# Kernel optimization log

Hardware: AMD Instinct MI355X
Metric: run time of the kernel (lower is better)

The kernel has to match this reference:

```python
import jax, jax.numpy as jnp
import numpy as np

B, N, H, OUT, T = 8192, 82, 10, 5, 3  # batch, n_nodes, hidden, output_channel, time_step


def setup_inputs() -> dict:
    key = jax.random.key(0)
    ks = jax.random.split(key, 20)

    def lin(kw, kb, fin, fout):
        w = jax.random.normal(kw, (fout, fin), jnp.float32) * (1.0 / np.sqrt(fin))
        b = jax.random.normal(kb, (fout,), jnp.float32) * 0.01
        return w, b

    w3w, b3w = lin(ks[0], ks[1], 2 * H, H)
    w3u, b3u = lin(ks[2], ks[3], H, H)
    w4w, b4w = lin(ks[4], ks[5], 2 * H, H)
    w5w, b5w = lin(ks[6], ks[7], 2 * H, H)
    w5u, b5u = lin(ks[8], ks[9], H, H)
    wout, bout = lin(ks[10], ks[11], 2 * H, OUT)
    return {
        'x': jax.random.normal(ks[12], (B, N, H), jnp.float32),
        'in_adj': jax.random.uniform(ks[13], (N, N), jnp.float32),
        'out_adj': jax.random.uniform(ks[14], (N, N), jnp.float32),
        'w3w': w3w, 'b3w': b3w, 'w3u': w3u, 'b3u': b3u,
        'w4w': w4w, 'b4w': b4w, 'w5w': w5w, 'b5w': b5w,
        'w5u': w5u, 'b5u': b5u, 'wout': wout, 'bout': bout,
    }


def _dense(v, w, b):
    return v @ w.T + b


def reference(x, in_adj, out_adj, w3w, b3w, w3u, b3u, w4w, b4w,
              w5w, b5w, w5u, b5u, wout, bout):
    b, n, h = x.shape
    nodes = x  # [B, N, H]
    fn = nodes.reshape(b * n, h)
    for _ in range(T):
        # neighbor aggregation; adjacency shared across batch (torch tiles it with repeat)
        a_in = jnp.einsum('ij,bjh->bih', in_adj, nodes)
        a_out = jnp.einsum('ij,bjh->bih', out_adj, nodes)
        av = jnp.concatenate([a_in, a_out], axis=-1).reshape(b * n, 2 * h)
        fn = nodes.reshape(b * n, h)
        zv = jax.nn.sigmoid(_dense(av, w3w, b3w) + _dense(fn, w3u, b3u))
        # NOTE: original torch code (bug) reuses fc_eq3_u here instead of fc_eq4_u
        rv = jax.nn.sigmoid(_dense(av, w4w, b4w) + _dense(fn, w3u, b3u))
        hv = jnp.tanh(_dense(av, w5w, b5w) + _dense(rv * fn, w5u, b5u))
        fn = (1.0 - zv) * fn + zv * hv
        nodes = fn.reshape(b, n, h)
    out_in = jnp.concatenate([fn, x.reshape(b * n, h)], axis=1)
    output = jnp.tanh(_dense(out_in, wout, bout))
    return output, fn
```

## Files before the change

kernel.cpp:

```cpp
#include <hip/hip_runtime.h>
#include <hip/hip_bf16.h>
#include <math.h>

#define B_TOTAL 8192
#define NN      82
#define HH      10
#define OUTC    5
#define TSTEP   3
#define NB      3
#define THREADS 256
#define KP      96
#define MP      16
#define XS      104
#define UTS     248

#define W3W 0
#define W4W 200
#define W5W 400
#define W3U 600
#define W5U 700
#define WOUT 800
#define B3W 900
#define B4W 910
#define B5W 920
#define B3U 930
#define B5U 940
#define BOUT 950
#define WTOT 960

typedef __bf16 bf16x8 __attribute__((ext_vector_type(8)));
typedef float  f32x4  __attribute__((ext_vector_type(4)));
typedef float  f32x2  __attribute__((ext_vector_type(2)));

__device__ __forceinline__ float sigmoid_(float x) {
    return 1.0f / (1.0f + __expf(-x));
}
__device__ __forceinline__ float tanh_(float x) {
    float e = __expf(2.0f * x);
    return 1.0f - 2.0f / (e + 1.0f);
}
__device__ __forceinline__ f32x2 ld2(const float* p) {
    return *reinterpret_cast<const f32x2*>(p);
}
__device__ __forceinline__ f32x2 fma2(f32x2 a, f32x2 b, f32x2 c) {
    return __builtin_elementwise_fma(a, b, c);
}

__global__ void prep_adj_kernel(const float* __restrict__ in_adj,
                                const float* __restrict__ out_adj,
                                __hip_bfloat16* __restrict__ adjP) {
    int idx = blockIdx.x * blockDim.x + threadIdx.x;
    if (idx < 2 * KP * KP) {
        int a   = idx / (KP * KP);
        int rem = idx - a * (KP * KP);
        int i = rem / KP;
        int j = rem - i * KP;
        float v = 0.0f;
        if (i < NN && j < NN) v = (a == 0) ? in_adj[i * NN + j] : out_adj[i * NN + j];
        __hip_bfloat16 hi = __float2bfloat16(v);
        __hip_bfloat16 lo = __float2bfloat16(v - __bfloat162float(hi));
        adjP[idx]               = hi;
        adjP[2 * KP * KP + idx] = lo;
    }
}

extern "C" __global__ __launch_bounds__(THREADS, 3)
void ggnn_kernel(const float* __restrict__ x,
                 const __hip_bfloat16* __restrict__ adjP,
                 const float* __restrict__ w3w, const float* __restrict__ b3w,
                 const float* __restrict__ w3u, const float* __restrict__ b3u,
                 const float* __restrict__ w4w, const float* __restrict__ b4w,
                 const float* __restrict__ w5w, const float* __restrict__ b5w,
                 const float* __restrict__ w5u, const float* __restrict__ b5u,
                 const float* __restrict__ wout, const float* __restrict__ bout,
                 float* __restrict__ out0, float* __restrict__ out_fn)
{
    __shared__ __align__(16) __hip_bfloat16 XtH[NB * MP][XS];
    __shared__ __align__(16) __hip_bfloat16 XtL[NB * MP][XS];
    __shared__ float uinT [HH][UTS];
    __shared__ float uoutT[HH][UTS];
    __shared__ __align__(16) float wS[WTOT];

    const int t     = threadIdx.x;
    const int bbase = blockIdx.x * NB;
    const int bl    = t / NN;
    const int node  = t - bl * NN;
    const bool act  = (bl < NB) && (bbase + bl < B_TOTAL);
    const int b     = bbase + bl;

    const int lane = t & 63;
    const int w    = t >> 6;
    const int lo16 = lane & 15;
    const int quad = lane >> 4;

    for (int i = t; i < 200; i += THREADS) {
        wS[W3W + i] = w3w[i];
        wS[W4W + i] = w4w[i];
        wS[W5W + i] = w5w[i];
    }
    if (t < 100) {
        wS[W3U + t]  = w3u[t];
        wS[W5U + t]  = w5u[t];
        wS[WOUT + t] = wout[t];
    }
    if (t < 10) {
        wS[B3W + t] = b3w[t];
        wS[B4W + t] = b4w[t];
        wS[B5W + t] = b5w[t];
        wS[B3U + t] = b3u[t];
        wS[B5U + t] = b5u[t];
    }
    if (t < OUTC) wS[BOUT + t] = bout[t];

    bf16x8 Bh[3][3], Bl[3][3];
    int ntile_c[3], adj_c[3];
    #pragma unroll
    for (int c = 0; c < 3; ++c) {
        int co = w * 3 + c;
        int nt = co >> 1;
        int ad = co & 1;
        ntile_c[c] = nt;
        adj_c[c]   = ad;
        const __hip_bfloat16* BpH = adjP + ((size_t)ad * KP * KP
                                            + (size_t)(nt * 16 + lo16) * KP
                                            + quad * 8);
        #pragma unroll
        for (int k = 0; k < 3; ++k) {
            Bh[c][k] = *reinterpret_cast<const bf16x8*>(BpH + k * 32);
            Bl[c][k] = *reinterpret_cast<const bf16x8*>(BpH + 2 * KP * KP + k * 32);
        }
    }

    for (int idx = t; idx < NB * NN * HH; idx += THREADS) {
        int b_l = idx / (NN * HH);
        int rem = idx - b_l * (NN * HH);
        int j   = rem / HH;
        int h   = rem - j * HH;
        size_t g = (size_t)bbase * NN * HH + idx;
        float v = (g < (size_t)B_TOTAL * NN * HH) ? x[g] : 0.0f;
        __hip_bfloat16 hi = __float2bfloat16(v);
        __hip_bfloat16 lo = __float2bfloat16(v - __bfloat162float(hi));
        XtH[b_l * MP + h][j] = hi;
        XtL[b_l * MP + h][j] = lo;
    }
    for (int idx = t; idx < NB * MP * (KP - NN); idx += THREADS) {
        int r = idx / (KP - NN);
        int c = idx - r * (KP - NN);
        __hip_bfloat16 z = __float2bfloat16(0.0f);
        XtH[r][NN + c] = z;
        XtL[r][NN + c] = z;
    }

    f32x2 fn2[5];
    if (act) {
        const float* xr = x + ((size_t)b * NN + node) * HH;
        #pragma unroll
        for (int p = 0; p < 5; ++p) {
            float2 v = reinterpret_cast<const float2*>(xr)[p];
            fn2[p].x = v.x; fn2[p].y = v.y;
        }
    }

    #pragma unroll 1
    for (int step = 0; step < TSTEP; ++step) {
        __syncthreads();

        #pragma unroll
        for (int mtile = 0; mtile < NB; ++mtile) {
            f32x4 acc[3] = {{0,0,0,0}, {0,0,0,0}, {0,0,0,0}};
            #pragma unroll
            for (int k = 0; k < 3; ++k) {
                bf16x8 ah = *reinterpret_cast<const bf16x8*>(&XtH[mtile * MP + lo16][quad * 8 + k * 32]);
                bf16x8 al = *reinterpret_cast<const bf16x8*>(&XtL[mtile * MP + lo16][quad * 8 + k * 32]);
                #pragma unroll
                for (int c = 0; c < 3; ++c) {
                    acc[c] = __builtin_amdgcn_mfma_f32_16x16x32_bf16(ah, Bh[c][k], acc[c], 0, 0, 0);
                    acc[c] = __builtin_amdgcn_mfma_f32_16x16x32_bf16(al, Bh[c][k], acc[c], 0, 0, 0);
                    acc[c] = __builtin_amdgcn_mfma_f32_16x16x32_bf16(ah, Bl[c][k], acc[c], 0, 0, 0);
                }
            }
            #pragma unroll
            for (int c = 0; c < 3; ++c) {
                int i = ntile_c[c] * 16 + lo16;
                if (i < NN) {
                    int col = mtile * NN + i;
                    float* plane0 = adj_c[c] ? &uoutT[0][0] : &uinT[0][0];
                    if (quad < 2) {
                        #pragma unroll
                        for (int r = 0; r < 4; ++r)
                            plane0[(quad * 4 + r) * UTS + col] = acc[c][r];
                    } else if (quad == 2) {
                        plane0[8 * UTS + col] = acc[c][0];
                        plane0[9 * UTS + col] = acc[c][1];
                    }
                }
            }
        }

        __syncthreads();

        if (act) {
            f32x2 av2[10];
            #pragma unroll
            for (int p = 0; p < 5; ++p) {
                av2[p].x     = uinT [2 * p][t];
                av2[p].y     = uinT [2 * p + 1][t];
                av2[5 + p].x = uoutT[2 * p][t];
                av2[5 + p].y = uoutT[2 * p + 1][t];
            }

            float u3[HH];
            #pragma unroll
            for (int h = 0; h < HH; ++h) {
                f32x2 s2 = {0.0f, 0.0f};
                #pragma unroll
                for (int p = 0; p < 5; ++p)
                    s2 = fma2(ld2(&wS[W3U + h * HH + 2 * p]), fn2[p], s2);
                u3[h] = wS[B3U + h] + s2.x + s2.y;
            }

            float zv[HH];
            f32x2 rf2[5];
            #pragma unroll
            for (int h = 0; h < HH; ++h) {
                f32x2 z2 = {0.0f, 0.0f}, r2 = {0.0f, 0.0f};
                #pragma unroll
                for (int p = 0; p < 10; ++p) {
                    z2 = fma2(ld2(&wS[W3W + h * 20 + 2 * p]), av2[p], z2);
                    r2 = fma2(ld2(&wS[W4W + h * 20 + 2 * p]), av2[p], r2);
                }
                zv[h] = sigmoid_(wS[B3W + h] + z2.x + z2.y + u3[h]);
                float rv = sigmoid_(wS[B4W + h] + r2.x + r2.y + u3[h]);
                float fnh = (h & 1) ? fn2[h >> 1].y : fn2[h >> 1].x;
                if (h & 1) rf2[h >> 1].y = rv * fnh; else rf2[h >> 1].x = rv * fnh;
            }

            #pragma unroll
            for (int h = 0; h < HH; ++h) {
                f32x2 s2 = {0.0f, 0.0f};
                #pragma unroll
                for (int p = 0; p < 10; ++p)
                    s2 = fma2(ld2(&wS[W5W + h * 20 + 2 * p]), av2[p], s2);
                #pragma unroll
                for (int p = 0; p < 5; ++p)
                    s2 = fma2(ld2(&wS[W5U + h * HH + 2 * p]), rf2[p], s2);
                float hv = tanh_(wS[B5W + h] + wS[B5U + h] + s2.x + s2.y);
                float fnh = (h & 1) ? fn2[h >> 1].y : fn2[h >> 1].x;
                fnh = fnh + zv[h] * (hv - fnh);
                if (h & 1) fn2[h >> 1].y = fnh; else fn2[h >> 1].x = fnh;
            }

            #pragma unroll
            for (int h = 0; h < HH; ++h) {
                float fnh = (h & 1) ? fn2[h >> 1].y : fn2[h >> 1].x;
                __hip_bfloat16 hi = __float2bfloat16(fnh);
                __hip_bfloat16 lo = __float2bfloat16(fnh - __bfloat162float(hi));
                XtH[bl * MP + h][node] = hi;
                XtL[bl * MP + h][node] = lo;
            }
        }
    }

    if (act) {
        size_t row = (size_t)b * NN + node;
        const float* xr = x + row * HH;
        f32x2 xi2[5];
        #pragma unroll
        for (int p = 0; p < 5; ++p) {
            float2 v = reinterpret_cast<const float2*>(xr)[p];
            xi2[p].x = v.x; xi2[p].y = v.y;
        }

        #pragma unroll
        for (int c = 0; c < OUTC; ++c) {
            f32x2 s2 = {0.0f, 0.0f};
            #pragma unroll
            for (int p = 0; p < 5; ++p) {
                s2 = fma2(ld2(&wS[WOUT + c * 20 + 2 * p]),      fn2[p], s2);
                s2 = fma2(ld2(&wS[WOUT + c * 20 + 10 + 2 * p]), xi2[p], s2);
            }
            out0[row * OUTC + c] = tanh_(wS[BOUT + c] + s2.x + s2.y);
        }
        #pragma unroll
        for (int p = 0; p < 5; ++p) {
            reinterpret_cast<float2*>(out_fn + row * HH)[p] =
                make_float2(fn2[p].x, fn2[p].y);
        }
    }
}

extern "C" void kernel_launch(void* const* d_in, const int* in_sizes, int n_in,
                              void* d_out, int out_size, void* d_ws, size_t ws_size,
                              hipStream_t stream) {
    const float* x       = (const float*)d_in[0];
    const float* in_adj  = (const float*)d_in[1];
    const float* out_adj = (const float*)d_in[2];
    const float* w3w = (const float*)d_in[3];
    const float* b3w = (const float*)d_in[4];
    const float* w3u = (const float*)d_in[5];
    const float* b3u = (const float*)d_in[6];
    const float* w4w = (const float*)d_in[7];
    const float* b4w = (const float*)d_in[8];
    const float* w5w = (const float*)d_in[9];
    const float* b5w = (const float*)d_in[10];
    const float* w5u = (const float*)d_in[11];
    const float* b5u = (const float*)d_in[12];
    const float* wout = (const float*)d_in[13];
    const float* bout = (const float*)d_in[14];

    __hip_bfloat16* adjP = (__hip_bfloat16*)d_ws;
    float* out0   = (float*)d_out;
    float* out_fn = out0 + (size_t)B_TOTAL * NN * OUTC;

    prep_adj_kernel<<<(2 * KP * KP + 255) / 256, 256, 0, stream>>>(in_adj, out_adj, adjP);

    int grid = (B_TOTAL + NB - 1) / NB;
    ggnn_kernel<<<grid, THREADS, 0, stream>>>(
        x, adjP, w3w, b3w, w3u, b3u, w4w, b4w, w5w, b5w, w5u, b5u,
        wout, bout, out0, out_fn);
}
```

Measured before the change: 264.6 us.

## Alias shared-memory buffers and pack batch rows to raise occupancy

Puts the bf16 X tiles and the float aggregation planes in one shared byte buffer that they take turns using, and shrinks the per-batch row pitch from 16 to 10. Extra barriers separate the MFMA reads, the aggregate writes and the av loads so the aliased regions do not collide. The accumulators for all m-tiles are now held in registers across the barrier. Launch bounds go from 3 to 6 blocks per CU to use the smaller LDS footprint. The trade-off is more __syncthreads and higher register pressure. The packed rows also make the MFMA A-loads read rows that belong to the neighbouring batch or are uninitialised, and that extra output is simply discarded. The pad-column zeroing has to be redone each step because the float planes overwrite it.

After: 684.0 us. 159% more time.

```diff
diff --git a/kernel.cpp b/kernel.cpp
--- a/kernel.cpp
+++ b/kernel.cpp
@@ -10,9 +10,14 @@
 #define NB      3
 #define THREADS 256
 #define KP      96
-#define MP      16
+#define RS      10
+#define NROWS   36
 #define XS      104
-#define UTS     248
+#define UTSF    246
+
+#define XTL_OFF 7488
+#define WS_OFF  19680
+#define SMEM_BYTES 23520
 
 #define W3W 0
 #define W4W 200
@@ -26,7 +31,6 @@
 #define B3U 930
 #define B5U 940
 #define BOUT 950
-#define WTOT 960
 
 typedef __bf16 bf16x8 __attribute__((ext_vector_type(8)));
 typedef float  f32x4  __attribute__((ext_vector_type(4)));
@@ -64,7 +68,7 @@
     }
 }
 
-extern "C" __global__ __launch_bounds__(THREADS, 3)
+extern "C" __global__ __launch_bounds__(THREADS, 6)
 void ggnn_kernel(const float* __restrict__ x,
                  const __hip_bfloat16* __restrict__ adjP,
                  const float* __restrict__ w3w, const float* __restrict__ b3w,
@@ -75,11 +79,11 @@
                  const float* __restrict__ wout, const float* __restrict__ bout,
                  float* __restrict__ out0, float* __restrict__ out_fn)
 {
-    __shared__ __align__(16) __hip_bfloat16 XtH[NB * MP][XS];
-    __shared__ __align__(16) __hip_bfloat16 XtL[NB * MP][XS];
-    __shared__ float uinT [HH][UTS];
-    __shared__ float uoutT[HH][UTS];
-    __shared__ __align__(16) float wS[WTOT];
+    __shared__ __align__(16) unsigned char smem[SMEM_BYTES];
+    __hip_bfloat16* XtH = reinterpret_cast<__hip_bfloat16*>(smem);
+    __hip_bfloat16* XtL = reinterpret_cast<__hip_bfloat16*>(smem + XTL_OFF);
+    float* uT = reinterpret_cast<float*>(smem);
+    float* wS = reinterpret_cast<float*>(smem + WS_OFF);
 
     const int t     = threadIdx.x;
     const int bbase = blockIdx.x * NB;
@@ -140,15 +144,18 @@
         float v = (g < (size_t)B_TOTAL * NN * HH) ? x[g] : 0.0f;
         __hip_bfloat16 hi = __float2bfloat16(v);
         __hip_bfloat16 lo = __float2bfloat16(v - __bfloat162float(hi));
-        XtH[b_l * MP + h][j] = hi;
-        XtL[b_l * MP + h][j] = lo;
-    }
-    for (int idx = t; idx < NB * MP * (KP - NN); idx += THREADS) {
-        int r = idx / (KP - NN);
-        int c = idx - r * (KP - NN);
+        XtH[(b_l * RS + h) * XS + j] = hi;
+        XtL[(b_l * RS + h) * XS + j] = lo;
+    }
+    {
         __hip_bfloat16 z = __float2bfloat16(0.0f);
-        XtH[r][NN + c] = z;
-        XtL[r][NN + c] = z;
+        for (int idx = t; idx < 2 * 30 * (KP - NN); idx += THREADS) {
+            int a   = idx / (30 * (KP - NN));
+            int rem = idx - a * (30 * (KP - NN));
+            int r   = rem / (KP - NN);
+            int c   = rem - r * (KP - NN);
+            (a ? XtL : XtH)[r * XS + NN + c] = z;
+        }
     }
 
     f32x2 fn2[5];
@@ -165,33 +172,41 @@
     for (int step = 0; step < TSTEP; ++step) {
         __syncthreads();
 
+        f32x4 acc[NB][3];
         #pragma unroll
         for (int mtile = 0; mtile < NB; ++mtile) {
-            f32x4 acc[3] = {{0,0,0,0}, {0,0,0,0}, {0,0,0,0}};
+            #pragma unroll
+            for (int c = 0; c < 3; ++c) acc[mtile][c] = (f32x4){0, 0, 0, 0};
             #pragma unroll
             for (int k = 0; k < 3; ++k) {
-                bf16x8 ah = *reinterpret_cast<const bf16x8*>(&XtH[mtile * MP + lo16][quad * 8 + k * 32]);
-                bf16x8 al = *reinterpret_cast<const bf16x8*>(&XtL[mtile * MP + lo16][quad * 8 + k * 32]);
+                bf16x8 ah = *reinterpret_cast<const bf16x8*>(&XtH[(mtile * RS + lo16) * XS + quad * 8 + k * 32]);
+                bf16x8 al = *reinterpret_cast<const bf16x8*>(&XtL[(mtile * RS + lo16) * XS + quad * 8 + k * 32]);
                 #pragma unroll
                 for (int c = 0; c < 3; ++c) {
-                    acc[c] = __builtin_amdgcn_mfma_f32_16x16x32_bf16(ah, Bh[c][k], acc[c], 0, 0, 0);
-                    acc[c] = __builtin_amdgcn_mfma_f32_16x16x32_bf16(al, Bh[c][k], acc[c], 0, 0, 0);
-                    acc[c] = __builtin_amdgcn_mfma_f32_16x16x32_bf16(ah, Bl[c][k], acc[c], 0, 0, 0);
+                    acc[mtile][c] = __builtin_amdgcn_mfma_f32_16x16x32_bf16(ah, Bh[c][k], acc[mtile][c], 0, 0, 0);
+                    acc[mtile][c] = __builtin_amdgcn_mfma_f32_16x16x32_bf16(al, Bh[c][k], acc[mtile][c], 0, 0, 0);
+                    acc[mtile][c] = __builtin_amdgcn_mfma_f32_16x16x32_bf16(ah, Bl[c][k], acc[mtile][c], 0, 0, 0);
                 }
             }
+        }
+
+        __syncthreads();
+
+        #pragma unroll
+        for (int mtile = 0; mtile < NB; ++mtile) {
             #pragma unroll
             for (int c = 0; c < 3; ++c) {
                 int i = ntile_c[c] * 16 + lo16;
                 if (i < NN) {
                     int col = mtile * NN + i;
-                    float* plane0 = adj_c[c] ? &uoutT[0][0] : &uinT[0][0];
+                    float* plane0 = uT + (adj_c[c] ? 10 * UTSF : 0);
                     if (quad < 2) {
                         #pragma unroll
                         for (int r = 0; r < 4; ++r)
-                            plane0[(quad * 4 + r) * UTS + col] = acc[c][r];
+                            plane0[(quad * 4 + r) * UTSF + col] = acc[mtile][c][r];
                     } else if (quad == 2) {
-                        plane0[8 * UTS + col] = acc[c][0];
-                        plane0[9 * UTS + col] = acc[c][1];
+                        plane0[8 * UTSF + col] = acc[mtile][c][0];
+                        plane0[9 * UTSF + col] = acc[mtile][c][1];
                     }
                 }
             }
@@ -199,16 +214,20 @@
 
         __syncthreads();
 
+        f32x2 av2[10];
         if (act) {
-            f32x2 av2[10];
             #pragma unroll
             for (int p = 0; p < 5; ++p) {
-                av2[p].x     = uinT [2 * p][t];
-                av2[p].y     = uinT [2 * p + 1][t];
-                av2[5 + p].x = uoutT[2 * p][t];
-                av2[5 + p].y = uoutT[2 * p + 1][t];
-            }
-
+                av2[p].x     = uT[(2 * p) * UTSF + t];
+                av2[p].y     = uT[(2 * p + 1) * UTSF + t];
+                av2[5 + p].x = uT[(10 + 2 * p) * UTSF + t];
+                av2[5 + p].y = uT[(10 + 2 * p + 1) * UTSF + t];
+            }
+        }
+
+        __syncthreads();
+
+        if (act) {
             float u3[HH];
             #pragma unroll
             for (int h = 0; h < HH; ++h) {
@@ -250,13 +269,25 @@
                 if (h & 1) fn2[h >> 1].y = fnh; else fn2[h >> 1].x = fnh;
             }
 
-            #pragma unroll
-            for (int h = 0; h < HH; ++h) {
-                float fnh = (h & 1) ? fn2[h >> 1].y : fn2[h >> 1].x;
-                __hip_bfloat16 hi = __float2bfloat16(fnh);
-                __hip_bfloat16 lo = __float2bfloat16(fnh - __bfloat162float(hi));
-                XtH[bl * MP + h][node] = hi;
-                XtL[bl * MP + h][node] = lo;
+            if (step < TSTEP - 1) {
+                #pragma unroll
+                for (int h = 0; h < HH; ++h) {
+                    float fnh = (h & 1) ? fn2[h >> 1].y : fn2[h >> 1].x;
+                    __hip_bfloat16 hi = __float2bfloat16(fnh);
+                    __hip_bfloat16 lo = __float2bfloat16(fnh - __bfloat162float(hi));
+                    XtH[(bl * RS + h) * XS + node] = hi;
+                    XtL[(bl * RS + h) * XS + node] = lo;
+                }
+            }
+        }
+        if (step < TSTEP - 1) {
+            __hip_bfloat16 z = __float2bfloat16(0.0f);
+            for (int idx = t; idx < 2 * 30 * (KP - NN); idx += THREADS) {
+                int a   = idx / (30 * (KP - NN));
+                int rem = idx - a * (30 * (KP - NN));
+                int r   = rem / (KP - NN);
+                int c   = rem - r * (KP - NN);
+                (a ? XtL : XtH)[r * XS + NN + c] = z;
             }
         }
     }
```
